# Performance work log

Hardware: AMD Instinct MI355X
Metric: run time of the kernel (lower is better)

The kernel has to match this reference:

```python
import jax, jax.numpy as jnp
import numpy as np

H = 512
IN_DIM = 300
NUM_CLASSES = 45
LN_EPS = 1e-5


def _ln(x, g, b):
    m = jnp.mean(x, axis=-1, keepdims=True)
    v = jnp.mean((x - m) ** 2, axis=-1, keepdims=True)
    return (x - m) / jnp.sqrt(v + LN_EPS) * g + b


def _rnn_dir(xemb, Wx, bx, Wh, bh, ln_g, ln_b):
    # xemb: [B, T, H]; Wx/Wh: [3, H, H]; bx/bh: [3, H]; ln_g/ln_b: [3, H]
    B = xemb.shape[0]
    h_init = (jnp.zeros((B, H), xemb.dtype),) * 3

    def step(carry, xt):
        h0, h1, h2 = carry
        h0 = jnp.tanh(_ln(xt @ Wx[0] + bx[0] + h0 @ Wh[0] + bh[0], ln_g[0], ln_b[0]))
        h1 = jnp.tanh(_ln(h0 @ Wx[1] + bx[1] + h1 @ Wh[1] + bh[1], ln_g[1], ln_b[1]))
        h2 = jnp.tanh(_ln(h1 @ Wx[2] + bx[2] + h2 @ Wh[2] + bh[2], ln_g[2], ln_b[2]))
        return (h0, h1, h2), h2

    _, ys = jax.lax.scan(step, h_init, jnp.swapaxes(xemb, 0, 1))  # ys: [T, B, H]
    return jnp.swapaxes(ys, 0, 1)  # [B, T, H]


def setup_inputs() -> dict:
    key = jax.random.key(0)
    ks = jax.random.split(key, 20)
    B, T = 128, 256
    s_in = 1.0 / np.sqrt(IN_DIM)
    s_h = 1.0 / np.sqrt(H)
    inp = {
        "x": jax.random.normal(ks[0], (B, T, IN_DIM), jnp.float32),
        "reverse_x": jax.random.normal(ks[1], (B, T, IN_DIM), jnp.float32),
        "pad_start_index": jax.random.randint(ks[2], (B,), 0, T),
        "max_length": T,
        "W_emb": jax.random.uniform(ks[3], (IN_DIM, H), jnp.float32, -s_in, s_in),
        "b_emb": jax.random.uniform(ks[4], (H,), jnp.float32, -s_in, s_in),
        "Wx_l2r": jax.random.uniform(ks[5], (3, H, H), jnp.float32, -s_h, s_h),
        "bx_l2r": jax.random.uniform(ks[6], (3, H), jnp.float32, -s_h, s_h),
        "Wh_l2r": jax.random.uniform(ks[7], (3, H, H), jnp.float32, -s_h, s_h),
        "bh_l2r": jax.random.uniform(ks[8], (3, H), jnp.float32, -s_h, s_h),
        "Wx_r2l": jax.random.uniform(ks[9], (3, H, H), jnp.float32, -s_h, s_h),
        "bx_r2l": jax.random.uniform(ks[10], (3, H), jnp.float32, -s_h, s_h),
        "Wh_r2l": jax.random.uniform(ks[11], (3, H, H), jnp.float32, -s_h, s_h),
        "bh_r2l": jax.random.uniform(ks[12], (3, H), jnp.float32, -s_h, s_h),
        "ln_g": jnp.ones((3, H), jnp.float32),
        "ln_b": jnp.zeros((3, H), jnp.float32),
        "W_fc": jax.random.uniform(ks[13], (2 * H, NUM_CLASSES), jnp.float32, -1.0 / np.sqrt(2 * H), 1.0 / np.sqrt(2 * H)),
        "b_fc": jax.random.uniform(ks[14], (NUM_CLASSES,), jnp.float32, -1.0 / np.sqrt(2 * H), 1.0 / np.sqrt(2 * H)),
    }
    return inp


def reference(x, reverse_x, pad_start_index, max_length, W_emb, b_emb,
              Wx_l2r, bx_l2r, Wh_l2r, bh_l2r, Wx_r2l, bx_r2l, Wh_r2l, bh_r2l,
              ln_g, ln_b, W_fc, b_fc):
    x = x[:, :max_length]
    reverse_x = reverse_x[:, :max_length]
    x_l2r = x @ W_emb + b_emb           # [B, T, H]
    x_r2l = reverse_x @ W_emb + b_emb
    out_l2r = _rnn_dir(x_l2r, Wx_l2r, bx_l2r, Wh_l2r, bh_l2r, ln_g, ln_b)
    out_r2l = _rnn_dir(x_r2l, Wx_r2l, bx_r2l, Wh_r2l, bh_r2l, ln_g, ln_b)
    T = out_l2r.shape[1]
    j = jnp.arange(T)[None, :]
    p = pad_start_index[:, None]
    idx = jnp.where(j < p, p - j - 1, j)  # [B, T] gather index into r2l time axis
    r2l_g = jnp.take_along_axis(out_r2l, idx[:, :, None], axis=1)
    concat = jnp.concatenate([out_l2r, r2l_g], axis=-1)  # [B, T, 2H]
    logit = concat @ W_fc + b_fc
    return logit.reshape(-1, logit.shape[-1])
```

## Files before the change

### kernel.cpp

```cpp
#include <hip/hip_runtime.h>

#define Bdim 128
#define Tdim 256
#define Hdim 512
#define INdim 300
#define KXdim 320
#define NC 45
#define NTHR 256
#define FPAD 16

typedef _Float16 h16;
typedef __attribute__((ext_vector_type(8))) _Float16 half8;
typedef __attribute__((ext_vector_type(4))) float float4v;
typedef unsigned long long u64;

__device__ __forceinline__ int ld_flag(const int* p) {
    return __hip_atomic_load((int*)p, __ATOMIC_RELAXED, __HIP_MEMORY_SCOPE_AGENT);
}
__device__ __forceinline__ void st_flag_rel(int* p, int v) {
    __hip_atomic_store(p, v, __ATOMIC_RELEASE, __HIP_MEMORY_SCOPE_AGENT);
}
__device__ __forceinline__ half8 ld16c(const h16* p) {
    union { u64 u[2]; half8 h; } r;
    const u64* q = (const u64*)p;
    r.u[0] = __hip_atomic_load((u64*)(q + 0), __ATOMIC_RELAXED, __HIP_MEMORY_SCOPE_AGENT);
    r.u[1] = __hip_atomic_load((u64*)(q + 1), __ATOMIC_RELAXED, __HIP_MEMORY_SCOPE_AGENT);
    return r.h;
}
__device__ __forceinline__ float4v ld16cf(const float* p) {
    union { u64 u[2]; float4v f; } r;
    const u64* q = (const u64*)p;
    r.u[0] = __hip_atomic_load((u64*)(q + 0), __ATOMIC_RELAXED, __HIP_MEMORY_SCOPE_AGENT);
    r.u[1] = __hip_atomic_load((u64*)(q + 1), __ATOMIC_RELAXED, __HIP_MEMORY_SCOPE_AGENT);
    return r.f;
}
__device__ __forceinline__ void st16cf(float* p, float4v v) {
    union { float4v f; u64 u[2]; } w; w.f = v;
    u64* q = (u64*)p;
    __hip_atomic_store(q + 0, w.u[0], __ATOMIC_RELAXED, __HIP_MEMORY_SCOPE_AGENT);
    __hip_atomic_store(q + 1, w.u[1], __ATOMIC_RELAXED, __HIP_MEMORY_SCOPE_AGENT);
}
__device__ __forceinline__ void st8c(h16* p, const uint* u) {
    uint* q = (uint*)p;
    __hip_atomic_store(q + 0, u[0], __ATOMIC_RELAXED, __HIP_MEMORY_SCOPE_AGENT);
    __hip_atomic_store(q + 1, u[1], __ATOMIC_RELAXED, __HIP_MEMORY_SCOPE_AGENT);
    __hip_atomic_store(q + 2, u[2], __ATOMIC_RELAXED, __HIP_MEMORY_SCOPE_AGENT);
    __hip_atomic_store(q + 3, u[3], __ATOMIC_RELAXED, __HIP_MEMORY_SCOPE_AGENT);
}

__device__ __forceinline__ half8 cvt_tanh(half8 zf, float A, float C,
                                          const float* g2, const float* b2)
{
    union { h16 h[8]; half8 v; } o;
    #pragma unroll
    for (int j = 0; j < 8; ++j) {
        float z = (float)zf[j];
        float x2 = __builtin_fmaf(__builtin_fmaf(z, A, C), g2[j], b2[j]);
        float E = __expf(x2);
        o.h[j] = (h16)(1.0f - __fdividef(2.0f, E + 1.0f));
    }
    return o.v;
}

__global__ __launch_bounds__(NTHR) void prep1_kernel(
    const float* Wemb, const float* bemb,
    const float* Wx_l2r, const float* bx_l2r, const float* bh_l2r,
    const float* Wx_r2l, const float* bx_r2l, const float* bh_r2l,
    float* W0, float* cb)
{
    int gid = blockIdx.x * NTHR + threadIdx.x;
    const int nW0 = 2 * KXdim * Hdim;
    if (gid < nW0) {
        int dir = gid / (KXdim * Hdim);
        int rem = gid % (KXdim * Hdim);
        int i = rem / Hdim, h = rem % Hdim;
        const float* Wx = dir ? Wx_r2l : Wx_l2r;
        float s = 0.f;
        if (i < INdim) {
            for (int k = 0; k < Hdim; ++k)
                s += Wemb[i * Hdim + k] * Wx[k * Hdim + h];
        }
        W0[gid] = s;
    } else {
        int idx = gid - nW0;
        if (idx < 2 * 3 * Hdim) {
            int dir = idx / (3 * Hdim);
            int l = (idx / Hdim) % 3;
            int h = idx % Hdim;
            const float* Wx = dir ? Wx_r2l : Wx_l2r;
            const float* bx = dir ? bx_r2l : bx_l2r;
            const float* bh = dir ? bh_r2l : bh_l2r;
            float s = bx[l * Hdim + h] + bh[l * Hdim + h];
            if (l == 0) {
                for (int k = 0; k < Hdim; ++k)
                    s += bemb[k] * Wx[k * Hdim + h];
            }
            cb[idx] = s;
        }
    }
}

__global__ __launch_bounds__(NTHR) void pack_W_kernel(
    const float* W0,
    const float* Wx_l2r, const float* Wh_l2r,
    const float* Wx_r2l, const float* Wh_r2l,
    h16* Wfrag)
{
    int e = blockIdx.x * NTHR + threadIdx.x;
    if (e >= 6 * 16 * 32 * 2 * 64 * 8) return;
    int j    = e & 7;
    int lane = (e >> 3) & 63;
    int nt   = (e >> 9) & 1;
    int ks   = (e >> 10) & 31;
    int cs   = (e >> 15) & 15;
    int u    = e >> 19;
    int dir = u / 3, l = u % 3;
    int n  = cs * 32 + nt * 16 + (lane & 15);
    int kk = ks * 32 + ((lane >> 4) * 8) + j;
    float v;
    if (kk < 512) {
        if (l == 0) {
            v = (kk < KXdim) ? W0[(dir * KXdim + kk) * Hdim + n] : 0.f;
        } else {
            const float* Wx = dir ? Wx_r2l : Wx_l2r;
            v = Wx[(l * Hdim + kk) * Hdim + n];
        }
    } else {
        const float* Wh = dir ? Wh_r2l : Wh_l2r;
        v = Wh[(l * Hdim + (kk - 512)) * Hdim + n];
    }
    Wfrag[e] = (h16)v;
}

__global__ __launch_bounds__(NTHR) void pack_W0f_kernel(const float* W0, h16* W0f)
{
    int e = blockIdx.x * NTHR + threadIdx.x;
    if (e >= 2 * 32 * 10 * 64 * 8) return;
    int j    = e & 7;
    int lane = (e >> 3) & 63;
    int rest = e >> 9;
    int ks   = rest % 10;
    rest /= 10;
    int nt   = rest & 31;
    int dir  = rest >> 5;
    int k = ks * 32 + ((lane >> 4) * 8) + j;
    int n = nt * 16 + (lane & 15);
    W0f[e] = (h16)W0[(dir * KXdim + k) * Hdim + n];
}

__global__ __launch_bounds__(NTHR) void zx0_kernel(
    const float* __restrict__ x0, const float* __restrict__ x1,
    const h16* __restrict__ W0f, const float* __restrict__ cb,
    h16* __restrict__ zx0f)
{
    int bx = blockIdx.x;
    int t = bx & 255, mh = (bx >> 8) & 1, dir = bx >> 9;
    const int tid = threadIdx.x;
    __shared__ h16 xl[64 * 328];
    const float* xs = dir ? x1 : x0;
    for (int i = tid; i < 64 * 328; i += NTHR) {
        int r = i / 328, k = i - r * 328;
        int b = mh * 64 + r;
        float v = (k < INdim) ? xs[(b * Tdim + t) * INdim + k] : 0.f;
        xl[i] = (h16)v;
    }
    __syncthreads();
    int wave = tid >> 6, lane = tid & 63;
    int r15 = lane & 15, q = lane >> 4;
    for (int nt = 0; nt < 32; ++nt) {
        float4v acc = {0.f, 0.f, 0.f, 0.f};
        #pragma unroll
        for (int ks = 0; ks < 10; ++ks) {
            half8 af = *(const half8*)&xl[(wave * 16 + r15) * 328 + ks * 32 + q * 8];
            half8 bf = *(const half8*)&W0f[(((dir * 32 + nt) * 10 + ks) * 64 + lane) * 8];
            acc = __builtin_amdgcn_mfma_f32_16x16x32_f16(af, bf, acc, 0, 0, 0);
        }
        int col = nt * 16 + r15;
        float cbv = cb[(dir * 3 + 0) * Hdim + col];
        union { h16 h[4]; uint2 u2; } o;
        #pragma unroll
        for (int r = 0; r < 4; ++r) o.h[r] = (h16)(acc[r] + cbv);
        h16* dst = zx0f + (((( (size_t)dir * Tdim + t) * 32 + nt) * 8 + (mh * 4 + wave)) * 64 + lane) * 4;
        *(uint2*)dst = o.u2;
    }
}

__global__ __launch_bounds__(NTHR) void zeroinit_kernel(int* zdoneH, int* zxdone)
{
    int gid = blockIdx.x * NTHR + threadIdx.x;
    if (gid < 6 * 32 * FPAD) zdoneH[gid] = 0;
    if (gid < 6 * 16 * FPAD) zxdone[gid] = 0;
}

struct PipeArgs {
    const h16* Wfrag;
    const h16* zx0f;
    const float* cb;
    const float* lng;
    const float* lnb;
    h16* zbuf;
    float* zxbuf;
    h16* h2;
    int* zdoneH;
    int* zxdone;
};

__global__ __launch_bounds__(NTHR, 1) void rnn_pipe(PipeArgs a)
{
    const int blk = blockIdx.x, tid = threadIdx.x;
    const int wave = tid >> 6, lane = tid & 63;
    const int r15 = lane & 15, quad = lane >> 4;
    const int u7 = blk & 7;

    __shared__ h16 wlds[32768];
    __shared__ float g2s[Hdim], b2s[Hdim];
    __shared__ h16 lds_z[64 * 32];

    if (u7 < 6) {
        const int u = u7, widx = blk >> 3;
        const int mtblk = widx & 1, cs = widx >> 1;
        const int dir = u / 3, l = u % 3;
        const int gmt = mtblk * 4 + wave;

        {
            const h16* src = a.Wfrag + (size_t)(u * 16 + cs) * 32768 + 16384;
            for (int i = tid * 8; i < 16384; i += NTHR * 8)
                *(uint4*)&wlds[i] = *(const uint4*)&src[i];
        }
        for (int i = tid; i < Hdim; i += NTHR) {
            g2s[i] = 2.0f * a.lng[l * Hdim + i];
            b2s[i] = 2.0f * a.lnb[l * Hdim + i];
        }
        __syncthreads();

        const int upperX = (u + 1) * 16 + mtblk * 8;
        const int zxflag = (u * 16 + mtblk * 8 + (cs >> 1)) * FPAD;

        for (int t = 0; t < Tdim; ++t) {
            for (;;) {
                int ok = 1;
                if (tid < 32) {
                    if (t > 0) ok = (ld_flag(&a.zdoneH[(u * 32 + tid) * FPAD]) >= t);
                } else if (tid >= 64 && tid < 72) {
                    if (l < 2 && t >= 4)
                        ok = (ld_flag(&a.zxdone[(upperX + tid - 64) * FPAD]) >= t - 3);
                }
                if (__syncthreads_and(ok)) break;
                __builtin_amdgcn_s_sleep(1);
            }
            asm volatile("" ::: "memory");

            float4v acc0 = {0.f, 0.f, 0.f, 0.f};
            float4v acc1 = {0.f, 0.f, 0.f, 0.f};
            if (t > 0) {
                const h16* zP = a.zbuf + (size_t)(u * 4 + ((t + 3) & 3)) * 65536;
                half8 af[16];
                #pragma unroll
                for (int ks = 0; ks < 16; ++ks)
                    af[ks] = ld16c(&zP[((ks * 8 + gmt) * 64 + lane) * 8]);
                float sm = 0.f, sq = 0.f;
                #pragma unroll
                for (int ks = 0; ks < 16; ++ks) {
                    #pragma unroll
                    for (int j = 0; j < 8; ++j) {
                        float v = (float)af[ks][j];
                        sm += v; sq = __builtin_fmaf(v, v, sq);
                    }
                }
                sm += __shfl_xor(sm, 16); sq += __shfl_xor(sq, 16);
                sm += __shfl_xor(sm, 32); sq += __shfl_xor(sq, 32);
                float m = sm * (1.0f / Hdim);
                float var = sq * (1.0f / Hdim) - m * m;
                float rstd = rsqrtf(var + 1e-5f);
                float A = rstd, Cc = -m * rstd;
                #pragma unroll
                for (int ks = 0; ks < 16; ++ks) {
                    int k0 = ks * 32 + quad * 8;
                    half8 hf = cvt_tanh(af[ks], A, Cc, &g2s[k0], &b2s[k0]);
                    if (l == 2 && ks == cs) {
                        union { half8 v; uint4 q; } w; w.v = hf;
                        *(uint4*)&a.h2[(((size_t)dir * Tdim + (t - 1)) * Bdim + gmt * 16 + r15) * Hdim + k0] = w.q;
                    }
                    half8 bh0 = *(const half8*)&wlds[((ks * 2 + 0) * 64 + lane) * 8];
                    half8 bh1 = *(const half8*)&wlds[((ks * 2 + 1) * 64 + lane) * 8];
                    acc0 = __builtin_amdgcn_mfma_f32_16x16x32_f16(hf, bh0, acc0, 0, 0, 0);
                    acc1 = __builtin_amdgcn_mfma_f32_16x16x32_f16(hf, bh1, acc1, 0, 0, 0);
                }
            }

            if (l > 0) {
                for (;;) {
                    int ok = 1;
                    if (tid < 32) ok = (ld_flag(&a.zxdone[zxflag]) >= t + 1);
                    if (__syncthreads_and(ok)) break;
                    __builtin_amdgcn_s_sleep(1);
                }
                asm volatile("" ::: "memory");
                const float* zx = a.zxbuf +
                    (((size_t)(u * 4 + (t & 3)) * 32 + cs * 2) * 8 + gmt) * 256 + lane * 4;
                float4v x0 = ld16cf(zx);
                float4v x1 = ld16cf(zx + 2048);
                acc0 += x0; acc1 += x1;
            } else {
                const h16* zp = a.zx0f +
                    (((((size_t)dir * Tdim + t) * 32 + cs * 2) * 8 + gmt) * 64 + lane) * 4;
                union { uint2 w; h16 h[4]; } v0, v1;
                v0.w = *(const uint2*)zp;
                v1.w = *(const uint2*)(zp + 2048);
                #pragma unroll
                for (int r = 0; r < 4; ++r) { acc0[r] += (float)v0.h[r]; acc1[r] += (float)v1.h[r]; }
            }

            #pragma unroll
            for (int r = 0; r < 4; ++r) {
                int lrow = wave * 16 + quad * 4 + r;
                lds_z[lrow * 32 + r15]      = (h16)acc0[r];
                lds_z[lrow * 32 + 16 + r15] = (h16)acc1[r];
            }
            __syncthreads();
            {
                int b_l = tid >> 2, c0 = (tid & 3) * 8;
                union { h16 h[8]; uint u4[4]; } o;
                const h16* srcz = &lds_z[b_l * 32 + c0];
                #pragma unroll
                for (int j = 0; j < 8; ++j) o.h[j] = srcz[j];
                int mt = mtblk * 4 + (b_l >> 4);
                int lane2 = (b_l & 15) | ((tid & 3) << 4);
                h16* dst = a.zbuf + (size_t)(u * 4 + (t & 3)) * 65536 +
                           ((size_t)((cs * 8 + mt) * 64 + lane2)) * 8;
                st8c(dst, o.u4);
            }
            __syncthreads();
            if (tid == 0) st_flag_rel(&a.zdoneH[(u * 32 + widx) * FPAD], t + 1);
        }

        if (l == 2) {
            for (;;) {
                int ok = 1;
                if (tid < 32) ok = (ld_flag(&a.zdoneH[(u * 32 + tid) * FPAD]) >= Tdim);
                if (__syncthreads_and(ok)) break;
                __builtin_amdgcn_s_sleep(1);
            }
            asm volatile("" ::: "memory");
            const h16* zP = a.zbuf + (size_t)(u * 4 + 3) * 65536;
            half8 af[16];
            #pragma unroll
            for (int ks = 0; ks < 16; ++ks)
                af[ks] = ld16c(&zP[((ks * 8 + gmt) * 64 + lane) * 8]);
            float sm = 0.f, sq = 0.f;
            #pragma unroll
            for (int ks = 0; ks < 16; ++ks) {
                #pragma unroll
                for (int j = 0; j < 8; ++j) {
                    float v = (float)af[ks][j];
                    sm += v; sq = __builtin_fmaf(v, v, sq);
                }
            }
            sm += __shfl_xor(sm, 16); sq += __shfl_xor(sq, 16);
            sm += __shfl_xor(sm, 32); sq += __shfl_xor(sq, 32);
            float m = sm * (1.0f / Hdim);
            float var = sq * (1.0f / Hdim) - m * m;
            float rstd = rsqrtf(var + 1e-5f);
            int k0 = cs * 32 + quad * 8;
            half8 hf = cvt_tanh(af[cs], rstd, -m * rstd, &g2s[k0], &b2s[k0]);
            union { half8 v; uint4 q; } w; w.v = hf;
            *(uint4*)&a.h2[(((size_t)dir * Tdim + (Tdim - 1)) * Bdim + gmt * 16 + r15) * Hdim + k0] = w.q;
        }
    } else {
        const int xraw = (blk >> 3) * 2 + (u7 - 6);
        const int xui = xraw >> 4;
        const int xu = (xui < 2) ? (xui + 1) : (xui + 2);
        const int sub = xraw & 15;
        const int mtblk = sub >> 3, cx = sub & 7;
        const int dir = xu / 3, l = xu % 3;
        const int lowU = xu - 1;
        const int gmt = mtblk * 4 + wave;

        {
            for (int f = tid; f < 4096; f += NTHR) {
                int ks = f >> 8;
                int rr = f & 255;
                int n  = rr >> 6;
                int li = rr & 63;
                int cs2 = 2 * cx + (n >> 1);
                int nt  = n & 1;
                const h16* src = a.Wfrag +
                    ((((size_t)(xu * 16 + cs2) * 32 + ks) * 2 + nt) * 64 + li) * 8;
                *(uint4*)&wlds[(size_t)f * 8] = *(const uint4*)src;
            }
        }
        for (int i = tid; i < Hdim; i += NTHR) {
            g2s[i] = 2.0f * a.lng[(l - 1) * Hdim + i];
            b2s[i] = 2.0f * a.lnb[(l - 1) * Hdim + i];
        }
        __syncthreads();

        float cbv[4];
        #pragma unroll
        for (int n = 0; n < 4; ++n)
            cbv[n] = a.cb[(dir * 3 + l) * Hdim + cx * 64 + n * 16 + r15];

        const int myflag = (xu * 16 + mtblk * 8 + cx) * FPAD;

        for (int t = 0; t < Tdim; ++t) {
            for (;;) {
                int ok = 1;
                if (tid < 32) {
                    ok = (ld_flag(&a.zdoneH[(lowU * 32 + tid) * FPAD]) >= t + 1);
                } else if (tid >= 64 && tid < 66) {
                    if (t >= 4) {
                        int wc = 4 * cx + mtblk + (tid - 64) * 2;
                        ok = (ld_flag(&a.zdoneH[(xu * 32 + wc) * FPAD]) >= t - 3);
                    }
                }
                if (__syncthreads_and(ok)) break;
                __builtin_amdgcn_s_sleep(1);
            }
            asm volatile("" ::: "memory");

            const h16* zP = a.zbuf + (size_t)(lowU * 4 + (t & 3)) * 65536;
            half8 af[16];
            #pragma unroll
            for (int ks = 0; ks < 16; ++ks)
                af[ks] = ld16c(&zP[((ks * 8 + gmt) * 64 + lane) * 8]);
            float sm = 0.f, sq = 0.f;
            #pragma unroll
            for (int ks = 0; ks < 16; ++ks) {
                #pragma unroll
                for (int j = 0; j < 8; ++j) {
                    float v = (float)af[ks][j];
                    sm += v; sq = __builtin_fmaf(v, v, sq);
                }
            }
            sm += __shfl_xor(sm, 16); sq += __shfl_xor(sq, 16);
            sm += __shfl_xor(sm, 32); sq += __shfl_xor(sq, 32);
            float m = sm * (1.0f / Hdim);
            float var = sq * (1.0f / Hdim) - m * m;
            float rstd = rsqrtf(var + 1e-5f);
            float A = rstd, Cc = -m * rstd;

            float4v acc[4];
            #pragma unroll
            for (int n = 0; n < 4; ++n) acc[n] = (float4v){0.f, 0.f, 0.f, 0.f};
            #pragma unroll
            for (int ks = 0; ks < 16; ++ks) {
                int k0 = ks * 32 + quad * 8;
                half8 hf = cvt_tanh(af[ks], A, Cc, &g2s[k0], &b2s[k0]);
                #pragma unroll
                for (int n = 0; n < 4; ++n) {
                    half8 bf = *(const half8*)&wlds[((ks * 4 + n) * 64 + lane) * 8];
                    acc[n] = __builtin_amdgcn_mfma_f32_16x16x32_f16(hf, bf, acc[n], 0, 0, 0);
                }
            }
            #pragma unroll
            for (int n = 0; n < 4; ++n) {
                float4v o = acc[n];
                #pragma unroll
                for (int r = 0; r < 4; ++r) o[r] += cbv[n];
                float* dst = a.zxbuf +
                    (((size_t)(xu * 4 + (t & 3)) * 32 + (cx * 4 + n)) * 8 + gmt) * 256 + lane * 4;
                st16cf(dst, o);
            }
            __syncthreads();
            if (tid == 0) st_flag_rel(&a.zxdone[myflag], t + 1);
        }
    }
}

__global__ __launch_bounds__(NTHR) void fc_kernel(
    const h16* __restrict__ h2, const int* __restrict__ pad,
    const float* __restrict__ Wfc, const float* __restrict__ bfc,
    float* __restrict__ out)
{
    __shared__ float sA[64 * 68];
    __shared__ float sB[64 * 48];
    const int blk = blockIdx.x, tid = threadIdx.x;
    const int b = blk >> 2;
    const int j0 = (blk & 3) * 64;
    const int p = pad[b];
    const int rg = tid >> 4;
    const int c0 = (tid & 15) * 3;
    float acc[4][3] = {};

    for (int k0 = 0; k0 < 2 * Hdim; k0 += 64) {
        {
            int rr = tid >> 2;
            int kp = (tid & 3) * 16;
            int j = j0 + rr;
            const h16* src;
            if (k0 < Hdim) {
                src = h2 + (((size_t)0 * Tdim + j) * Bdim + b) * Hdim + k0 + kp;
            } else {
                int idx = (j < p) ? (p - j - 1) : j;
                src = h2 + (((size_t)1 * Tdim + idx) * Bdim + b) * Hdim + (k0 - Hdim) + kp;
            }
            union { uint4 u4; h16 h[8]; } w0, w1;
            w0.u4 = *(const uint4*)src;
            w1.u4 = *(const uint4*)(src + 8);
            #pragma unroll
            for (int i = 0; i < 8; ++i) {
                sA[rr * 68 + kp + i]     = (float)w0.h[i];
                sA[rr * 68 + kp + 8 + i] = (float)w1.h[i];
            }
        }
        for (int e = tid; e < 64 * 48; e += NTHR) {
            int kk = e / 48, c = e - kk * 48;
            sB[e] = (c < NC) ? Wfc[(k0 + kk) * NC + c] : 0.f;
        }
        __syncthreads();
        for (int kk = 0; kk < 64; ++kk) {
            float b0 = sB[kk * 48 + c0 + 0];
            float b1 = sB[kk * 48 + c0 + 1];
            float b2 = sB[kk * 48 + c0 + 2];
            #pragma unroll
            for (int i = 0; i < 4; ++i) {
                float av = sA[(rg * 4 + i) * 68 + kk];
                acc[i][0] += av * b0; acc[i][1] += av * b1; acc[i][2] += av * b2;
            }
        }
        __syncthreads();
    }
    #pragma unroll
    for (int i = 0; i < 4; ++i) {
        int r = blk * 64 + rg * 4 + i;
        #pragma unroll
        for (int jj = 0; jj < 3; ++jj) {
            int c = c0 + jj;
            if (c < NC) out[r * NC + c] = acc[i][jj] + bfc[c];
        }
    }
}

extern "C" void kernel_launch(void* const* d_in, const int* in_sizes, int n_in,
                              void* d_out, int out_size, void* d_ws, size_t ws_size,
                              hipStream_t stream) {
    const float* x      = (const float*)d_in[0];
    const float* rx     = (const float*)d_in[1];
    const int*   pad    = (const int*)d_in[2];
    const float* Wemb   = (const float*)d_in[4];
    const float* bemb   = (const float*)d_in[5];
    const float* Wx_l2r = (const float*)d_in[6];
    const float* bx_l2r = (const float*)d_in[7];
    const float* Wh_l2r = (const float*)d_in[8];
    const float* bh_l2r = (const float*)d_in[9];
    const float* Wx_r2l = (const float*)d_in[10];
    const float* bx_r2l = (const float*)d_in[11];
    const float* Wh_r2l = (const float*)d_in[12];
    const float* bh_r2l = (const float*)d_in[13];
    const float* lng    = (const float*)d_in[14];
    const float* lnb    = (const float*)d_in[15];
    const float* Wfc    = (const float*)d_in[16];
    const float* bfc    = (const float*)d_in[17];

    char* base = (char*)d_ws;
    size_t off = 0;
    auto alloc = [&](size_t bytes) { char* p = base + off; off += (bytes + 255) & ~(size_t)255; return p; };
    h16*   zx0f  = (h16*)  alloc((size_t)2 * Tdim * 32 * 8 * 64 * 4 * 2);
    h16*   h2    = (h16*)  alloc((size_t)2 * Tdim * Bdim * Hdim * 2);
    h16*   Wfrag = (h16*)  alloc((size_t)6 * 16 * 32768 * 2);
    h16*   W0f   = (h16*)  alloc((size_t)2 * 32 * 10 * 64 * 8 * 2);
    h16*   zbuf  = (h16*)  alloc((size_t)6 * 4 * 65536 * 2);
    float* zxbuf = (float*)alloc((size_t)6 * 4 * 32 * 8 * 64 * 4 * 4);
    float* W0    = (float*)alloc((size_t)2 * KXdim * Hdim * 4);
    float* cb    = (float*)alloc((size_t)2 * 3 * Hdim * 4);
    int*   zdoneH = (int*) alloc((size_t)6 * 32 * FPAD * 4);
    int*   zxdone = (int*) alloc((size_t)6 * 16 * FPAD * 4);

    prep1_kernel<<<(2 * KXdim * Hdim + 2 * 3 * Hdim) / NTHR, NTHR, 0, stream>>>(
        Wemb, bemb, Wx_l2r, bx_l2r, bh_l2r, Wx_r2l, bx_r2l, bh_r2l, W0, cb);

    pack_W_kernel<<<(6 * 16 * 32 * 2 * 64 * 8) / NTHR, NTHR, 0, stream>>>(
        W0, Wx_l2r, Wh_l2r, Wx_r2l, Wh_r2l, Wfrag);

    pack_W0f_kernel<<<(2 * 32 * 10 * 64 * 8) / NTHR, NTHR, 0, stream>>>(W0, W0f);

    zx0_kernel<<<1024, NTHR, 0, stream>>>(x, rx, W0f, cb, zx0f);

    zeroinit_kernel<<<(6 * 32 * FPAD + NTHR - 1) / NTHR, NTHR, 0, stream>>>(zdoneH, zxdone);

    PipeArgs a;
    a.Wfrag = Wfrag; a.zx0f = zx0f; a.cb = cb; a.lng = lng; a.lnb = lnb;
    a.zbuf = zbuf; a.zxbuf = zxbuf; a.h2 = h2;
    a.zdoneH = zdoneH; a.zxdone = zxdone;
    void* kargs[] = { &a };
    hipLaunchCooperativeKernel((void*)rnn_pipe, dim3(256), dim3(NTHR), kargs, 0, stream);

    fc_kernel<<<(Bdim * Tdim) / 64, NTHR, 0, stream>>>(h2, pad, Wfc, bfc, (float*)d_out);
}
```

Measured before the change: 3.597 ms.

## Restructure RNN pipeline: fewer recurrent blocks each owning 64 rows with local LayerNorm

```diff
diff --git a/kernel.cpp b/kernel.cpp
--- a/kernel.cpp
+++ b/kernel.cpp
@@ -7,6 +7,7 @@
 #define KXdim 320
 #define NC 45
 #define NTHR 256
+#define NH 512
 #define FPAD 16
 
 typedef _Float16 h16;
@@ -46,20 +47,6 @@
     __hip_atomic_store(q + 1, u[1], __ATOMIC_RELAXED, __HIP_MEMORY_SCOPE_AGENT);
     __hip_atomic_store(q + 2, u[2], __ATOMIC_RELAXED, __HIP_MEMORY_SCOPE_AGENT);
     __hip_atomic_store(q + 3, u[3], __ATOMIC_RELAXED, __HIP_MEMORY_SCOPE_AGENT);
-}
-
-__device__ __forceinline__ half8 cvt_tanh(half8 zf, float A, float C,
-                                          const float* g2, const float* b2)
-{
-    union { h16 h[8]; half8 v; } o;
-    #pragma unroll
-    for (int j = 0; j < 8; ++j) {
-        float z = (float)zf[j];
-        float x2 = __builtin_fmaf(__builtin_fmaf(z, A, C), g2[j], b2[j]);
-        float E = __expf(x2);
-        o.h[j] = (h16)(1.0f - __fdividef(2.0f, E + 1.0f));
-    }
-    return o.v;
 }
 
 __global__ __launch_bounds__(NTHR) void prep1_kernel(
@@ -185,11 +172,11 @@
     }
 }
 
-__global__ __launch_bounds__(NTHR) void zeroinit_kernel(int* zdoneH, int* zxdone)
+__global__ __launch_bounds__(NTHR) void zeroinit_kernel(int* hdone, int* zxdone)
 {
     int gid = blockIdx.x * NTHR + threadIdx.x;
-    if (gid < 6 * 32 * FPAD) zdoneH[gid] = 0;
-    if (gid < 6 * 16 * FPAD) zxdone[gid] = 0;
+    if (gid < 12 * FPAD) hdone[gid] = 0;
+    if (gid < 96 * FPAD) zxdone[gid] = 0;
 }
 
 struct PipeArgs {
@@ -198,269 +185,291 @@
     const float* cb;
     const float* lng;
     const float* lnb;
-    h16* zbuf;
+    h16* hbuf;
     float* zxbuf;
     h16* h2;
-    int* zdoneH;
+    int* hdone;
     int* zxdone;
 };
 
-__global__ __launch_bounds__(NTHR, 1) void rnn_pipe(PipeArgs a)
-{
+struct HS {
+    h16 h[64 * 536];
+    float red_s[8][64];
+    float red_q[8][64];
+    float mr[64][2];
+    float g2b2[512][2];
+};
+struct XS { h16 wx[16 * 4 * 64 * 8]; };
+union SMem { HS H; XS X; };
+
+__global__ __launch_bounds__(NH, 2) void rnn_pipe(PipeArgs a)
+{
+    __shared__ SMem sm;
     const int blk = blockIdx.x, tid = threadIdx.x;
-    const int wave = tid >> 6, lane = tid & 63;
+    const int w4 = tid >> 6, lane = tid & 63;
     const int r15 = lane & 15, quad = lane >> 4;
-    const int u7 = blk & 7;
-
-    __shared__ h16 wlds[32768];
-    __shared__ float g2s[Hdim], b2s[Hdim];
-    __shared__ h16 lds_z[64 * 32];
-
-    if (u7 < 6) {
-        const int u = u7, widx = blk >> 3;
-        const int mtblk = widx & 1, cs = widx >> 1;
+
+    if (blk < 12) {
+        const int u = blk >> 1, mtblk = blk & 1;
         const int dir = u / 3, l = u % 3;
-        const int gmt = mtblk * 4 + wave;
-
-        {
-            const h16* src = a.Wfrag + (size_t)(u * 16 + cs) * 32768 + 16384;
-            for (int i = tid * 8; i < 16384; i += NTHR * 8)
-                *(uint4*)&wlds[i] = *(const uint4*)&src[i];
-        }
-        for (int i = tid; i < Hdim; i += NTHR) {
-            g2s[i] = 2.0f * a.lng[l * Hdim + i];
-            b2s[i] = 2.0f * a.lnb[l * Hdim + i];
+
+        for (int i = tid; i < Hdim; i += NH) {
+            sm.H.g2b2[i][0] = 2.0f * a.lng[l * Hdim + i];
+            sm.H.g2b2[i][1] = 2.0f * a.lnb[l * Hdim + i];
         }
         __syncthreads();
 
-        const int upperX = (u + 1) * 16 + mtblk * 8;
-        const int zxflag = (u * 16 + mtblk * 8 + (cs >> 1)) * FPAD;
+        const int loff = lane * 8;
+        const h16* wbase[4];
+        #pragma unroll
+        for (int n = 0; n < 4; ++n) {
+            int ntg = w4 * 4 + n;
+            wbase[n] = a.Wfrag + (((size_t)(u * 16 + (ntg >> 1)) * 32 + 16) * 2 + (ntg & 1)) * 512;
+        }
+
+        float4v acc[4][4];
+
+        auto convert = [&](int tm1) {
+            float s16[4][4], q16[4][4];
+            #pragma unroll
+            for (int mt = 0; mt < 4; ++mt)
+                #pragma unroll
+                for (int r = 0; r < 4; ++r) { s16[mt][r] = 0.f; q16[mt][r] = 0.f; }
+            #pragma unroll
+            for (int mt = 0; mt < 4; ++mt)
+                #pragma unroll
+                for (int n = 0; n < 4; ++n)
+                    #pragma unroll
+                    for (int r = 0; r < 4; ++r) {
+                        float v = acc[mt][n][r];
+                        s16[mt][r] += v;
+                        q16[mt][r] = __builtin_fmaf(v, v, q16[mt][r]);
+                    }
+            #pragma unroll
+            for (int mt = 0; mt < 4; ++mt)
+                #pragma unroll
+                for (int r = 0; r < 4; ++r) {
+                    float s = s16[mt][r], q = q16[mt][r];
+                    s += __shfl_xor(s, 1); q += __shfl_xor(q, 1);
+                    s += __shfl_xor(s, 2); q += __shfl_xor(q, 2);
+                    s += __shfl_xor(s, 4); q += __shfl_xor(q, 4);
+                    s += __shfl_xor(s, 8); q += __shfl_xor(q, 8);
+                    s16[mt][r] = s; q16[mt][r] = q;
+                }
+            if (r15 == 0) {
+                #pragma unroll
+                for (int mt = 0; mt < 4; ++mt)
+                    #pragma unroll
+                    for (int r = 0; r < 4; ++r) {
+                        int row = mt * 16 + quad * 4 + r;
+                        sm.H.red_s[w4][row] = s16[mt][r];
+                        sm.H.red_q[w4][row] = q16[mt][r];
+                    }
+            }
+            __syncthreads();
+            if (tid < 64) {
+                float ss = 0.f, qq = 0.f;
+                #pragma unroll
+                for (int ww = 0; ww < 8; ++ww) { ss += sm.H.red_s[ww][tid]; qq += sm.H.red_q[ww][tid]; }
+                float m = ss * (1.0f / Hdim);
+                float var = qq * (1.0f / Hdim) - m * m;
+                float rstd = rsqrtf(var + 1e-5f);
+                sm.H.mr[tid][0] = rstd;
+                sm.H.mr[tid][1] = -m * rstd;
+            }
+            __syncthreads();
+            float rA[4][4], rC[4][4];
+            #pragma unroll
+            for (int mt = 0; mt < 4; ++mt)
+                #pragma unroll
+                for (int r = 0; r < 4; ++r) {
+                    int row = mt * 16 + quad * 4 + r;
+                    rA[mt][r] = sm.H.mr[row][0];
+                    rC[mt][r] = sm.H.mr[row][1];
+                }
+            float gg[4], bg[4];
+            #pragma unroll
+            for (int n = 0; n < 4; ++n) {
+                int col = (w4 * 4 + n) * 16 + r15;
+                gg[n] = sm.H.g2b2[col][0];
+                bg[n] = sm.H.g2b2[col][1];
+            }
+            #pragma unroll
+            for (int mt = 0; mt < 4; ++mt)
+                #pragma unroll
+                for (int n = 0; n < 4; ++n)
+                    #pragma unroll
+                    for (int r = 0; r < 4; ++r) {
+                        float x2 = __builtin_fmaf(
+                            __builtin_fmaf(acc[mt][n][r], rA[mt][r], rC[mt][r]), gg[n], bg[n]);
+                        float E = __expf(x2);
+                        sm.H.h[(mt * 16 + quad * 4 + r) * 536 + (w4 * 4 + n) * 16 + r15] =
+                            (h16)(1.0f - __fdividef(2.0f, E + 1.0f));
+                    }
+            __syncthreads();
+            if (l < 2) {
+                h16* dstb = a.hbuf + (size_t)(u * 4 + (tm1 & 3)) * 65536;
+                #pragma unroll
+                for (int i = 0; i < 8; ++i) {
+                    int f = tid + i * NH;
+                    int ks = f >> 8, mt4 = (f >> 6) & 3, ln = f & 63;
+                    union { half8 v; uint uu[4]; } o;
+                    o.v = *(const half8*)&sm.H.h[(mt4 * 16 + (ln & 15)) * 536 + ks * 32 + (ln >> 4) * 8];
+                    st8c(dstb + ((size_t)((ks * 8 + (mtblk * 4 + mt4)) * 64) + ln) * 8, o.uu);
+                }
+            } else {
+                int row = tid >> 3, cseg = (tid & 7) * 64;
+                h16* d2 = a.h2 + (((size_t)dir * Tdim + tm1) * Bdim + mtblk * 64 + row) * Hdim + cseg;
+                #pragma unroll
+                for (int i = 0; i < 8; ++i)
+                    *(uint4*)(d2 + i * 8) = *(const uint4*)&sm.H.h[row * 536 + cseg + i * 8];
+            }
+        };
 
         for (int t = 0; t < Tdim; ++t) {
-            for (;;) {
-                int ok = 1;
-                if (tid < 32) {
-                    if (t > 0) ok = (ld_flag(&a.zdoneH[(u * 32 + tid) * FPAD]) >= t);
-                } else if (tid >= 64 && tid < 72) {
-                    if (l < 2 && t >= 4)
-                        ok = (ld_flag(&a.zxdone[(upperX + tid - 64) * FPAD]) >= t - 3);
-                }
-                if (__syncthreads_and(ok)) break;
-                __builtin_amdgcn_s_sleep(1);
-            }
-            asm volatile("" ::: "memory");
-
-            float4v acc0 = {0.f, 0.f, 0.f, 0.f};
-            float4v acc1 = {0.f, 0.f, 0.f, 0.f};
-            if (t > 0) {
-                const h16* zP = a.zbuf + (size_t)(u * 4 + ((t + 3) & 3)) * 65536;
-                half8 af[16];
-                #pragma unroll
-                for (int ks = 0; ks < 16; ++ks)
-                    af[ks] = ld16c(&zP[((ks * 8 + gmt) * 64 + lane) * 8]);
-                float sm = 0.f, sq = 0.f;
-                #pragma unroll
-                for (int ks = 0; ks < 16; ++ks) {
-                    #pragma unroll
-                    for (int j = 0; j < 8; ++j) {
-                        float v = (float)af[ks][j];
-                        sm += v; sq = __builtin_fmaf(v, v, sq);
-                    }
-                }
-                sm += __shfl_xor(sm, 16); sq += __shfl_xor(sq, 16);
-                sm += __shfl_xor(sm, 32); sq += __shfl_xor(sq, 32);
-                float m = sm * (1.0f / Hdim);
-                float var = sq * (1.0f / Hdim) - m * m;
-                float rstd = rsqrtf(var + 1e-5f);
-                float A = rstd, Cc = -m * rstd;
-                #pragma unroll
-                for (int ks = 0; ks < 16; ++ks) {
-                    int k0 = ks * 32 + quad * 8;
-                    half8 hf = cvt_tanh(af[ks], A, Cc, &g2s[k0], &b2s[k0]);
-                    if (l == 2 && ks == cs) {
-                        union { half8 v; uint4 q; } w; w.v = hf;
-                        *(uint4*)&a.h2[(((size_t)dir * Tdim + (t - 1)) * Bdim + gmt * 16 + r15) * Hdim + k0] = w.q;
-                    }
-                    half8 bh0 = *(const half8*)&wlds[((ks * 2 + 0) * 64 + lane) * 8];
-                    half8 bh1 = *(const half8*)&wlds[((ks * 2 + 1) * 64 + lane) * 8];
-                    acc0 = __builtin_amdgcn_mfma_f32_16x16x32_f16(hf, bh0, acc0, 0, 0, 0);
-                    acc1 = __builtin_amdgcn_mfma_f32_16x16x32_f16(hf, bh1, acc1, 0, 0, 0);
-                }
-            }
-
-            if (l > 0) {
+            if (l < 2 && t >= 5) {
                 for (;;) {
                     int ok = 1;
-                    if (tid < 32) ok = (ld_flag(&a.zxdone[zxflag]) >= t + 1);
+                    if (tid >= 64 && tid < 72)
+                        ok = (ld_flag(&a.zxdone[((u + 1) * 16 + mtblk * 8 + (tid - 64)) * FPAD]) >= t - 4);
                     if (__syncthreads_and(ok)) break;
                     __builtin_amdgcn_s_sleep(1);
                 }
                 asm volatile("" ::: "memory");
-                const float* zx = a.zxbuf +
-                    (((size_t)(u * 4 + (t & 3)) * 32 + cs * 2) * 8 + gmt) * 256 + lane * 4;
-                float4v x0 = ld16cf(zx);
-                float4v x1 = ld16cf(zx + 2048);
-                acc0 += x0; acc1 += x1;
+            }
+            if (t > 0) {
+                convert(t - 1);
+                #pragma unroll
+                for (int mt = 0; mt < 4; ++mt)
+                    #pragma unroll
+                    for (int n = 0; n < 4; ++n)
+                        acc[mt][n] = (float4v){0.f, 0.f, 0.f, 0.f};
+                #pragma unroll
+                for (int ks = 0; ks < 16; ++ks) {
+                    half8 af[4], bf[4];
+                    #pragma unroll
+                    for (int mt = 0; mt < 4; ++mt)
+                        af[mt] = *(const half8*)&sm.H.h[(mt * 16 + r15) * 536 + ks * 32 + quad * 8];
+                    #pragma unroll
+                    for (int n = 0; n < 4; ++n)
+                        bf[n] = *(const half8*)&wbase[n][ks * 1024 + loff];
+                    #pragma unroll
+                    for (int mt = 0; mt < 4; ++mt)
+                        #pragma unroll
+                        for (int n = 0; n < 4; ++n)
+                            acc[mt][n] = __builtin_amdgcn_mfma_f32_16x16x32_f16(af[mt], bf[n], acc[mt][n], 0, 0, 0);
+                }
+                __syncthreads();
+                if (tid == 0) st_flag_rel(&a.hdone[(u * 2 + mtblk) * FPAD], t);
             } else {
-                const h16* zp = a.zx0f +
-                    (((((size_t)dir * Tdim + t) * 32 + cs * 2) * 8 + gmt) * 64 + lane) * 4;
-                union { uint2 w; h16 h[4]; } v0, v1;
-                v0.w = *(const uint2*)zp;
-                v1.w = *(const uint2*)(zp + 2048);
-                #pragma unroll
-                for (int r = 0; r < 4; ++r) { acc0[r] += (float)v0.h[r]; acc1[r] += (float)v1.h[r]; }
-            }
-
-            #pragma unroll
-            for (int r = 0; r < 4; ++r) {
-                int lrow = wave * 16 + quad * 4 + r;
-                lds_z[lrow * 32 + r15]      = (h16)acc0[r];
-                lds_z[lrow * 32 + 16 + r15] = (h16)acc1[r];
-            }
-            __syncthreads();
-            {
-                int b_l = tid >> 2, c0 = (tid & 3) * 8;
-                union { h16 h[8]; uint u4[4]; } o;
-                const h16* srcz = &lds_z[b_l * 32 + c0];
-                #pragma unroll
-                for (int j = 0; j < 8; ++j) o.h[j] = srcz[j];
-                int mt = mtblk * 4 + (b_l >> 4);
-                int lane2 = (b_l & 15) | ((tid & 3) << 4);
-                h16* dst = a.zbuf + (size_t)(u * 4 + (t & 3)) * 65536 +
-                           ((size_t)((cs * 8 + mt) * 64 + lane2)) * 8;
-                st8c(dst, o.u4);
-            }
-            __syncthreads();
-            if (tid == 0) st_flag_rel(&a.zdoneH[(u * 32 + widx) * FPAD], t + 1);
-        }
-
-        if (l == 2) {
+                #pragma unroll
+                for (int mt = 0; mt < 4; ++mt)
+                    #pragma unroll
+                    for (int n = 0; n < 4; ++n)
+                        acc[mt][n] = (float4v){0.f, 0.f, 0.f, 0.f};
+            }
+            if (l > 0) {
+                for (;;) {
+                    int ok = 1;
+                    if (tid < 8) ok = (ld_flag(&a.zxdone[(u * 16 + mtblk * 8 + tid) * FPAD]) >= t + 1);
+                    if (__syncthreads_and(ok)) break;
+                    __builtin_amdgcn_s_sleep(1);
+                }
+                asm volatile("" ::: "memory");
+                const float* zxb = a.zxbuf + (size_t)(u * 4 + (t & 3)) * 65536;
+                #pragma unroll
+                for (int mt = 0; mt < 4; ++mt)
+                    #pragma unroll
+                    for (int n = 0; n < 4; ++n) {
+                        int ntg = w4 * 4 + n, gmt = mtblk * 4 + mt;
+                        float4v xv = ld16cf(zxb + ((size_t)(ntg * 8 + gmt) * 64 + lane) * 4);
+                        acc[mt][n] += xv;
+                    }
+            } else {
+                #pragma unroll
+                for (int mt = 0; mt < 4; ++mt)
+                    #pragma unroll
+                    for (int n = 0; n < 4; ++n) {
+                        int ntg = w4 * 4 + n, gmt = mtblk * 4 + mt;
+                        const h16* zp = a.zx0f + ((((size_t)dir * Tdim + t) * 32 + ntg) * 8 + gmt) * 256 + lane * 4;
+                        union { uint2 uu; h16 hh[4]; } vv;
+                        vv.uu = *(const uint2*)zp;
+                        #pragma unroll
+                        for (int r = 0; r < 4; ++r) acc[mt][n][r] += (float)vv.hh[r];
+                    }
+            }
+        }
+        if (l < 2) {
             for (;;) {
                 int ok = 1;
-                if (tid < 32) ok = (ld_flag(&a.zdoneH[(u * 32 + tid) * FPAD]) >= Tdim);
+                if (tid >= 64 && tid < 72)
+                    ok = (ld_flag(&a.zxdone[((u + 1) * 16 + mtblk * 8 + (tid - 64)) * FPAD]) >= Tdim - 4);
                 if (__syncthreads_and(ok)) break;
                 __builtin_amdgcn_s_sleep(1);
             }
             asm volatile("" ::: "memory");
-            const h16* zP = a.zbuf + (size_t)(u * 4 + 3) * 65536;
-            half8 af[16];
-            #pragma unroll
-            for (int ks = 0; ks < 16; ++ks)
-                af[ks] = ld16c(&zP[((ks * 8 + gmt) * 64 + lane) * 8]);
-            float sm = 0.f, sq = 0.f;
-            #pragma unroll
-            for (int ks = 0; ks < 16; ++ks) {
-                #pragma unroll
-                for (int j = 0; j < 8; ++j) {
-                    float v = (float)af[ks][j];
-                    sm += v; sq = __builtin_fmaf(v, v, sq);
-                }
-            }
-            sm += __shfl_xor(sm, 16); sq += __shfl_xor(sq, 16);
-            sm += __shfl_xor(sm, 32); sq += __shfl_xor(sq, 32);
-            float m = sm * (1.0f / Hdim);
-            float var = sq * (1.0f / Hdim) - m * m;
-            float rstd = rsqrtf(var + 1e-5f);
-            int k0 = cs * 32 + quad * 8;
-            half8 hf = cvt_tanh(af[cs], rstd, -m * rstd, &g2s[k0], &b2s[k0]);
-            union { half8 v; uint4 q; } w; w.v = hf;
-            *(uint4*)&a.h2[(((size_t)dir * Tdim + (Tdim - 1)) * Bdim + gmt * 16 + r15) * Hdim + k0] = w.q;
-        }
+        }
+        convert(Tdim - 1);
+        __syncthreads();
+        if (tid == 0) st_flag_rel(&a.hdone[(u * 2 + mtblk) * FPAD], Tdim);
     } else {
-        const int xraw = (blk >> 3) * 2 + (u7 - 6);
-        const int xui = xraw >> 4;
+        const int xi = blk - 12;
+        const int xui = xi >> 4;
         const int xu = (xui < 2) ? (xui + 1) : (xui + 2);
-        const int sub = xraw & 15;
-        const int mtblk = sub >> 3, cx = sub & 7;
+        const int sub = xi & 15, mtblk = sub >> 3, cx = sub & 7;
         const int dir = xu / 3, l = xu % 3;
-        const int lowU = xu - 1;
-        const int gmt = mtblk * 4 + wave;
-
-        {
-            for (int f = tid; f < 4096; f += NTHR) {
-                int ks = f >> 8;
-                int rr = f & 255;
-                int n  = rr >> 6;
-                int li = rr & 63;
-                int cs2 = 2 * cx + (n >> 1);
-                int nt  = n & 1;
-                const h16* src = a.Wfrag +
-                    ((((size_t)(xu * 16 + cs2) * 32 + ks) * 2 + nt) * 64 + li) * 8;
-                *(uint4*)&wlds[(size_t)f * 8] = *(const uint4*)src;
-            }
-        }
-        for (int i = tid; i < Hdim; i += NTHR) {
-            g2s[i] = 2.0f * a.lng[(l - 1) * Hdim + i];
-            b2s[i] = 2.0f * a.lnb[(l - 1) * Hdim + i];
+        const int gmt = mtblk * 4 + (w4 & 3);
+        const int npair = w4 >> 2;
+
+        #pragma unroll
+        for (int i = 0; i < 8; ++i) {
+            int f = tid + i * NH;
+            int ks = f >> 8, ntl = (f >> 6) & 3, ln = f & 63;
+            int ntg = cx * 4 + ntl;
+            const h16* src = a.Wfrag + (((size_t)(xu * 16 + (ntg >> 1)) * 32 + ks) * 2 + (ntg & 1)) * 512 + ln * 8;
+            *(uint4*)&sm.X.wx[((size_t)(ks * 4 + ntl) * 64 + ln) * 8] = *(const uint4*)src;
         }
         __syncthreads();
 
-        float cbv[4];
+        float cbv[2];
         #pragma unroll
-        for (int n = 0; n < 4; ++n)
-            cbv[n] = a.cb[(dir * 3 + l) * Hdim + cx * 64 + n * 16 + r15];
-
-        const int myflag = (xu * 16 + mtblk * 8 + cx) * FPAD;
+        for (int n = 0; n < 2; ++n) {
+            int col = (cx * 4 + npair * 2 + n) * 16 + r15;
+            cbv[n] = a.cb[(dir * 3 + l) * Hdim + col];
+        }
+        const int loflag  = ((xu - 1) * 2 + mtblk) * FPAD;
+        const int thrflag = (xu * 2 + mtblk) * FPAD;
+        const int myflag  = (xu * 16 + mtblk * 8 + cx) * FPAD;
 
         for (int t = 0; t < Tdim; ++t) {
             for (;;) {
                 int ok = 1;
-                if (tid < 32) {
-                    ok = (ld_flag(&a.zdoneH[(lowU * 32 + tid) * FPAD]) >= t + 1);
-                } else if (tid >= 64 && tid < 66) {
-                    if (t >= 4) {
-                        int wc = 4 * cx + mtblk + (tid - 64) * 2;
-                        ok = (ld_flag(&a.zdoneH[(xu * 32 + wc) * FPAD]) >= t - 3);
-                    }
-                }
+                if (tid == 0) ok = (ld_flag(&a.hdone[loflag]) >= t + 1);
+                else if (tid == 64 && t >= 4) ok = (ld_flag(&a.hdone[thrflag]) >= t - 3);
                 if (__syncthreads_and(ok)) break;
                 __builtin_amdgcn_s_sleep(1);
             }
             asm volatile("" ::: "memory");
 
-            const h16* zP = a.zbuf + (size_t)(lowU * 4 + (t & 3)) * 65536;
+            const h16* hb = a.hbuf + (size_t)((xu - 1) * 4 + (t & 3)) * 65536;
             half8 af[16];
             #pragma unroll
             for (int ks = 0; ks < 16; ++ks)
-                af[ks] = ld16c(&zP[((ks * 8 + gmt) * 64 + lane) * 8]);
-            float sm = 0.f, sq = 0.f;
+                af[ks] = ld16c(&hb[((size_t)(ks * 8 + gmt) * 64 + lane) * 8]);
+            float4v a0 = {0.f, 0.f, 0.f, 0.f}, a1 = {0.f, 0.f, 0.f, 0.f};
             #pragma unroll
             for (int ks = 0; ks < 16; ++ks) {
-                #pragma unroll
-                for (int j = 0; j < 8; ++j) {
-                    float v = (float)af[ks][j];
-                    sm += v; sq = __builtin_fmaf(v, v, sq);
-                }
-            }
-            sm += __shfl_xor(sm, 16); sq += __shfl_xor(sq, 16);
-            sm += __shfl_xor(sm, 32); sq += __shfl_xor(sq, 32);
-            float m = sm * (1.0f / Hdim);
-            float var = sq * (1.0f / Hdim) - m * m;
-            float rstd = rsqrtf(var + 1e-5f);
-            float A = rstd, Cc = -m * rstd;
-
-            float4v acc[4];
-            #pragma unroll
-            for (int n = 0; n < 4; ++n) acc[n] = (float4v){0.f, 0.f, 0.f, 0.f};
-            #pragma unroll
-            for (int ks = 0; ks < 16; ++ks) {
-                int k0 = ks * 32 + quad * 8;
-                half8 hf = cvt_tanh(af[ks], A, Cc, &g2s[k0], &b2s[k0]);
-                #pragma unroll
-                for (int n = 0; n < 4; ++n) {
-                    half8 bf = *(const half8*)&wlds[((ks * 4 + n) * 64 + lane) * 8];
-                    acc[n] = __builtin_amdgcn_mfma_f32_16x16x32_f16(hf, bf, acc[n], 0, 0, 0);
-                }
-            }
-            #pragma unroll
-            for (int n = 0; n < 4; ++n) {
-                float4v o = acc[n];
-                #pragma unroll
-                for (int r = 0; r < 4; ++r) o[r] += cbv[n];
-                float* dst = a.zxbuf +
-                    (((size_t)(xu * 4 + (t & 3)) * 32 + (cx * 4 + n)) * 8 + gmt) * 256 + lane * 4;
-                st16cf(dst, o);
-            }
+                half8 b0 = *(const half8*)&sm.X.wx[((size_t)(ks * 4 + npair * 2 + 0) * 64 + lane) * 8];
+                half8 b1 = *(const half8*)&sm.X.wx[((size_t)(ks * 4 + npair * 2 + 1) * 64 + lane) * 8];
+                a0 = __builtin_amdgcn_mfma_f32_16x16x32_f16(af[ks], b0, a0, 0, 0, 0);
+                a1 = __builtin_amdgcn_mfma_f32_16x16x32_f16(af[ks], b1, a1, 0, 0, 0);
+            }
+            #pragma unroll
+            for (int r = 0; r < 4; ++r) { a0[r] += cbv[0]; a1[r] += cbv[1]; }
+            float* zxb = a.zxbuf + (size_t)(xu * 4 + (t & 3)) * 65536;
+            int n0 = cx * 4 + npair * 2;
+            st16cf(zxb + ((size_t)((n0 + 0) * 8 + gmt) * 64 + lane) * 4, a0);
+            st16cf(zxb + ((size_t)((n0 + 1) * 8 + gmt) * 64 + lane) * 4, a1);
             __syncthreads();
             if (tid == 0) st_flag_rel(&a.zxdone[myflag], t + 1);
         }
@@ -559,12 +568,12 @@
     h16*   h2    = (h16*)  alloc((size_t)2 * Tdim * Bdim * Hdim * 2);
     h16*   Wfrag = (h16*)  alloc((size_t)6 * 16 * 32768 * 2);
     h16*   W0f   = (h16*)  alloc((size_t)2 * 32 * 10 * 64 * 8 * 2);
-    h16*   zbuf  = (h16*)  alloc((size_t)6 * 4 * 65536 * 2);
-    float* zxbuf = (float*)alloc((size_t)6 * 4 * 32 * 8 * 64 * 4 * 4);
+    h16*   hbuf  = (h16*)  alloc((size_t)6 * 4 * 65536 * 2);
+    float* zxbuf = (float*)alloc((size_t)6 * 4 * 65536 * 4);
     float* W0    = (float*)alloc((size_t)2 * KXdim * Hdim * 4);
     float* cb    = (float*)alloc((size_t)2 * 3 * Hdim * 4);
-    int*   zdoneH = (int*) alloc((size_t)6 * 32 * FPAD * 4);
-    int*   zxdone = (int*) alloc((size_t)6 * 16 * FPAD * 4);
+    int*   hdone  = (int*) alloc((size_t)12 * FPAD * 4);
+    int*   zxdone = (int*) alloc((size_t)96 * FPAD * 4);
 
     prep1_kernel<<<(2 * KXdim * Hdim + 2 * 3 * Hdim) / NTHR, NTHR, 0, stream>>>(
         Wemb, bemb, Wx_l2r, bx_l2r, bh_l2r, Wx_r2l, bx_r2l, bh_r2l, W0, cb);
@@ -576,14 +585,14 @@
 
     zx0_kernel<<<1024, NTHR, 0, stream>>>(x, rx, W0f, cb, zx0f);
 
-    zeroinit_kernel<<<(6 * 32 * FPAD + NTHR - 1) / NTHR, NTHR, 0, stream>>>(zdoneH, zxdone);
+    zeroinit_kernel<<<(96 * FPAD + NTHR - 1) / NTHR, NTHR, 0, stream>>>(hdone, zxdone);
 
     PipeArgs a;
     a.Wfrag = Wfrag; a.zx0f = zx0f; a.cb = cb; a.lng = lng; a.lnb = lnb;
-    a.zbuf = zbuf; a.zxbuf = zxbuf; a.h2 = h2;
-    a.zdoneH = zdoneH; a.zxdone = zxdone;
+    a.hbuf = hbuf; a.zxbuf = zxbuf; a.h2 = h2;
+    a.hdone = hdone; a.zxdone = zxdone;
     void* kargs[] = { &a };
-    hipLaunchCooperativeKernel((void*)rnn_pipe, dim3(256), dim3(NTHR), kargs, 0, stream);
+    hipLaunchCooperativeKernel((void*)rnn_pipe, dim3(76), dim3(NH), kargs, 0, stream);
 
     fc_kernel<<<(Bdim * Tdim) / 64, NTHR, 0, stream>>>(h2, pad, Wfc, bfc, (float*)d_out);
 }
```

Measured after the change: 7.523 ms. 2.09x slower.
